# Performance work log

Hardware: AMD Instinct MI355X
Metric: run time of the kernel (lower is better)

## Reference

```python
import jax, jax.numpy as jnp
import numpy as np

DIM = 1024
HEADS = 16
HEAD_DIM = DIM // HEADS
EPS = 1e-5


def setup_inputs() -> dict:
    key = jax.random.key(0)
    ks = jax.random.split(key, 4)
    N, L = 4, 2048
    x = jax.random.normal(ks[0], (N, L, DIM), dtype=jnp.float32)
    # causal mask: True means masked (strictly upper triangle)
    attn_mask = jnp.triu(jnp.ones((L, L), dtype=jnp.bool_), k=1)[None, None, :, :]
    w_qkv = jax.random.normal(ks[1], (3 * DIM, DIM), dtype=jnp.float32) * (DIM ** -0.5)
    w_proj = jax.random.normal(ks[2], (DIM, DIM), dtype=jnp.float32) * (DIM ** -0.5)
    b_proj = jnp.zeros((DIM,), dtype=jnp.float32)
    q_gamma = jnp.ones((HEAD_DIM,), dtype=jnp.float32)
    q_beta = jnp.zeros((HEAD_DIM,), dtype=jnp.float32)
    k_gamma = jnp.ones((HEAD_DIM,), dtype=jnp.float32)
    k_beta = jnp.zeros((HEAD_DIM,), dtype=jnp.float32)
    return {"x": x, "attn_mask": attn_mask, "w_qkv": w_qkv, "w_proj": w_proj,
            "b_proj": b_proj, "q_gamma": q_gamma, "q_beta": q_beta,
            "k_gamma": k_gamma, "k_beta": k_beta}


def _layernorm(h, gamma, beta):
    mu = jnp.mean(h, axis=-1, keepdims=True)
    var = jnp.mean(jnp.square(h - mu), axis=-1, keepdims=True)
    return (h - mu) * jax.lax.rsqrt(var + EPS) * gamma + beta


def reference(x, attn_mask, w_qkv, w_proj, b_proj, q_gamma, q_beta, k_gamma, k_beta):
    N, L, D = x.shape
    H, hd = HEADS, HEAD_DIM
    scale = hd ** -0.5
    qkv = jnp.einsum('nld,ed->nle', x, w_qkv)  # [N, L, 3D]
    qkv = qkv.reshape(N, L, 3, H, hd).transpose(2, 0, 3, 1, 4)  # [3, N, H, L, hd]
    q, k, v = qkv[0], qkv[1], qkv[2]
    q = _layernorm(q, q_gamma, q_beta)
    k = _layernorm(k, k_gamma, k_beta)
    scores = jnp.einsum('nhqd,nhkd->nhqk', q * scale, k)
    scores = scores + jnp.where(attn_mask, -jnp.inf, 0.0).astype(scores.dtype)
    attn = jax.nn.softmax(scores, axis=-1)
    out = jnp.einsum('nhqk,nhkd->nhqd', attn, v)  # [N, H, L, hd]
    out = out.transpose(0, 2, 1, 3).reshape(N, L, D)
    return jnp.einsum('nld,ed->nle', out, w_proj) + b_proj
```

## Files before the change

### kernel.cpp

```cpp
#include <hip/hip_runtime.h>


using f16x8 = __attribute__((ext_vector_type(8))) _Float16;
using f16x4 = __attribute__((ext_vector_type(4))) _Float16;
using f16x2 = __attribute__((ext_vector_type(2))) _Float16;
using f32x4 = __attribute__((ext_vector_type(4))) float;
using f32x16 = __attribute__((ext_vector_type(16))) float;
using u32x4 = __attribute__((ext_vector_type(4))) unsigned int;

#define MFMA16(a, b, c) __builtin_amdgcn_mfma_f32_16x16x32_f16(a, b, c, 0, 0, 0)
#define MFMA32(a, b, c) __builtin_amdgcn_mfma_f32_32x32x16_f16(a, b, c, 0, 0, 0)

__device__ __forceinline__ void gload_lds16(const void* g, void* l) {
  __builtin_amdgcn_global_load_lds(
      (const __attribute__((address_space(1))) unsigned int*)g,
      (__attribute__((address_space(3))) unsigned int*)l, 16, 0, 0);
}

__device__ __forceinline__ float dot2acc(unsigned int pk, float c) {
#if __has_builtin(__builtin_amdgcn_fdot2)
  const f16x2 ones = {(_Float16)1.f, (_Float16)1.f};
  return __builtin_amdgcn_fdot2(__builtin_bit_cast(f16x2, pk), ones, c, false);
#else
  f16x2 v = __builtin_bit_cast(f16x2, pk);
  return c + (float)v[0] + (float)v[1];
#endif
}

__global__ __launch_bounds__(256) void f32_to_f16_kernel(
    const float* __restrict__ in, _Float16* __restrict__ out, int n) {
  int i = (blockIdx.x * 256 + threadIdx.x) * 8;
  if (i >= n) return;
  float4 a = *(const float4*)(in + i);
  float4 b = *(const float4*)(in + i + 4);
  f16x8 o;
  o[0] = (_Float16)a.x; o[1] = (_Float16)a.y; o[2] = (_Float16)a.z; o[3] = (_Float16)a.w;
  o[4] = (_Float16)b.x; o[5] = (_Float16)b.y; o[6] = (_Float16)b.z; o[7] = (_Float16)b.w;
  *(f16x8*)(out + i) = o;
}

template <int MODE>
__global__ __launch_bounds__(256) void gemm_bt(
    const _Float16* __restrict__ A, const _Float16* __restrict__ B,
    void* __restrict__ Cout, _Float16* __restrict__ Vt,
    const float* __restrict__ bias,
    const float* __restrict__ qg, const float* __restrict__ qb,
    const float* __restrict__ kg, const float* __restrict__ kb,
    int M, int N, int K) {
  __shared__ __align__(16) _Float16 As[128 * 32];
  __shared__ __align__(16) _Float16 Bs[128 * 32];
  const int tid = threadIdx.x;
  const int w = tid >> 6, lane = tid & 63;
  const int c = lane & 15, g = lane >> 4;
  const long mbase = (long)blockIdx.x * 128;
  const long nbase = (long)blockIdx.y * 128;
  const int wm = (w >> 1) * 64, wn = (w & 1) * 64;
  const int srow = w * 32 + (lane >> 2);
  const int scol = (lane & 3) * 8;

  f32x4 acc[4][4];
#pragma unroll
  for (int i = 0; i < 4; ++i)
#pragma unroll
    for (int j = 0; j < 4; ++j) acc[i][j] = f32x4{0.f, 0.f, 0.f, 0.f};

  for (int kt = 0; kt < K; kt += 32) {
    __syncthreads();
    gload_lds16(A + (mbase + srow) * K + kt + scol, As + w * 1024);
    gload_lds16(A + (mbase + srow + 16) * K + kt + scol, As + w * 1024 + 512);
    gload_lds16(B + (nbase + srow) * K + kt + scol, Bs + w * 1024);
    gload_lds16(B + (nbase + srow + 16) * K + kt + scol, Bs + w * 1024 + 512);
    __syncthreads();
    f16x8 af[4], bfr[4];
#pragma unroll
    for (int mt = 0; mt < 4; ++mt)
      af[mt] = *(const f16x8*)(As + (wm + mt * 16 + c) * 32 + g * 8);
#pragma unroll
    for (int nt = 0; nt < 4; ++nt)
      bfr[nt] = *(const f16x8*)(Bs + (wn + nt * 16 + c) * 32 + g * 8);
#pragma unroll
    for (int mt = 0; mt < 4; ++mt)
#pragma unroll
      for (int nt = 0; nt < 4; ++nt)
        acc[mt][nt] = MFMA16(af[mt], bfr[nt], acc[mt][nt]);
  }

  if constexpr (MODE == 1) {
    const int region = (int)(nbase >> 10);
    if (region == 2) {
#pragma unroll
      for (int nt = 0; nt < 4; ++nt) {
        const int dg = (int)(nbase + wn) + nt * 16 + c - 2048;
        const long vrow = ((mbase >> 11) * 16 + (dg >> 6)) * 64 + (dg & 63);
#pragma unroll
        for (int mt = 0; mt < 4; ++mt) {
          const long l0 = (mbase & 2047) + wm + mt * 16 + g * 4;
          f16x4 o;
#pragma unroll
          for (int r = 0; r < 4; ++r) o[r] = (_Float16)acc[mt][nt][r];
          *(f16x4*)(Vt + vrow * 2048 + l0) = o;
        }
      }
      return;
    }
    const float* gamma = region ? kg : qg;
    const float* beta = region ? kb : qb;
    float gam[4], bet[4];
#pragma unroll
    for (int nt = 0; nt < 4; ++nt) {
      gam[nt] = gamma[nt * 16 + c];
      bet[nt] = beta[nt * 16 + c];
    }
    const float sc = region ? 1.f : 0.1803368801111204f;
#pragma unroll
    for (int mt = 0; mt < 4; ++mt)
#pragma unroll
      for (int r = 0; r < 4; ++r) {
        float s1 = 0.f, s2 = 0.f;
#pragma unroll
        for (int nt = 0; nt < 4; ++nt) {
          const float v = acc[mt][nt][r];
          s1 += v;
          s2 += v * v;
        }
#pragma unroll
        for (int msk = 1; msk < 16; msk <<= 1) {
          s1 += __shfl_xor(s1, msk);
          s2 += __shfl_xor(s2, msk);
        }
        const float mu = s1 * 0.015625f;
        const float rstd = rsqrtf(s2 * 0.015625f - mu * mu + 1e-5f);
#pragma unroll
        for (int nt = 0; nt < 4; ++nt)
          acc[mt][nt][r] =
              ((acc[mt][nt][r] - mu) * rstd * gam[nt] + bet[nt]) * sc;
      }
#pragma unroll
    for (int nt = 0; nt < 4; ++nt) {
      const long col = nbase + wn + nt * 16 + c;
#pragma unroll
      for (int mt = 0; mt < 4; ++mt)
#pragma unroll
        for (int r = 0; r < 4; ++r) {
          const long row = mbase + wm + mt * 16 + g * 4 + r;
          ((_Float16*)Cout)[row * N + col] = (_Float16)acc[mt][nt][r];
        }
    }
  } else {
#pragma unroll
    for (int nt = 0; nt < 4; ++nt) {
      const long col = nbase + wn + nt * 16 + c;
      const float bv = bias ? bias[col] : 0.f;
#pragma unroll
      for (int mt = 0; mt < 4; ++mt)
#pragma unroll
        for (int r = 0; r < 4; ++r) {
          const long row = mbase + wm + mt * 16 + g * 4 + r;
          ((float*)Cout)[row * N + col] = acc[mt][nt][r] + bv;
        }
    }
  }
}

__global__ __launch_bounds__(256) void attn_kernel(
    const _Float16* __restrict__ qkv, const _Float16* __restrict__ Vt,
    _Float16* __restrict__ Ob) {
  __shared__ __align__(16) _Float16 Ks[2][64 * 64];
  __shared__ __align__(16) _Float16 Vs[2][64 * 64];
  const int w = threadIdx.x >> 6;
  const int lane = threadIdx.x & 63;
  const int c5 = lane & 31;
  const int hi = lane >> 5;
  const int nh = blockIdx.x;
  const long n = nh >> 4;
  const int h = nh & 15;
  const int qtile = 15 - blockIdx.y;
  const int qlo_blk = qtile * 128;
  const int qlo = qlo_blk + w * 32;
  const int qrow = qlo + c5;

  const _Float16* Qp = qkv + n * 2048 * 3072 + h * 64;
  const _Float16* Kq = Qp + 1024;
  const _Float16* Vp = Vt + (long)nh * 64 * 2048;

  const int sr8 = lane >> 3;
  const int scol = ((lane & 7) ^ sr8) * 8;

  const int nkv_blk = (qlo_blk + 191) >> 6;
  const int nkv_w = (qlo + 95) >> 6;

  const float NEG_M = -12.0f;

#define STAGE(buf, kv)                                                        \
  {                                                                           \
    const int kb_ = (kv) * 64;                                                \
    _Pragma("unroll") for (int i = 0; i < 2; ++i) {                           \
      const int idx = w * 2 + i;                                              \
      const int row = idx * 8 + sr8;                                          \
      gload_lds16(Kq + (long)(kb_ + row) * 3072 + scol, &Ks[buf][idx * 512]); \
      gload_lds16(Vp + (long)row * 2048 + kb_ + scol, &Vs[buf][idx * 512]);   \
    }                                                                         \
  }

  f16x8 qf[4];
#pragma unroll
  for (int dc = 0; dc < 4; ++dc)
    qf[dc] = *(const f16x8*)(Qp + (long)qrow * 3072 + dc * 16 + hi * 8);

  f32x16 acc[2];
#pragma unroll
  for (int db = 0; db < 2; ++db)
#pragma unroll
    for (int r = 0; r < 16; ++r) acc[db][r] = 0.f;
  float ls = 0.f;

  STAGE(0, 0);

  const int swr = c5 & 7;

  for (int kv = 0; kv < nkv_blk; ++kv) {
    const int cur = kv & 1;
    __syncthreads();
    if (kv + 1 < nkv_blk) STAGE(cur ^ 1, kv + 1);

    if (kv < nkv_w) {
      const int kbase = kv * 64;
      const _Float16* Kb = Ks[cur];
      const _Float16* Vb = Vs[cur];
      f32x16 s0, s1;
#pragma unroll
      for (int r = 0; r < 16; ++r) { s0[r] = NEG_M; s1[r] = NEG_M; }
      __builtin_amdgcn_s_setprio(1);
#pragma unroll
      for (int dc = 0; dc < 4; ++dc) {
        const int b = (dc * 2 + hi) ^ swr;
        f16x8 kf0 = *(const f16x8*)(Kb + c5 * 64 + b * 8);
        f16x8 kf1 = *(const f16x8*)(Kb + (32 + c5) * 64 + b * 8);
        s0 = MFMA32(kf0, qf[dc], s0);
        s1 = MFMA32(kf1, qf[dc], s1);
      }
      __builtin_amdgcn_s_setprio(0);
      if (kbase + 63 > qlo) {
#pragma unroll
        for (int r = 0; r < 16; ++r) {
          const int mv = (r & 3) + 8 * (r >> 2) + 4 * hi;
          if (kbase + mv > qrow) s0[r] = -1e30f;
          if (kbase + 32 + mv > qrow) s1[r] = -1e30f;
        }
      }
#pragma unroll
      for (int r = 0; r < 16; ++r) {
        s0[r] = exp2f(s0[r]);
        s1[r] = exp2f(s1[r]);
      }
      unsigned int pk0[4][2], pk1[4][2];
#pragma unroll
      for (int r2 = 0; r2 < 4; ++r2)
#pragma unroll
        for (int p = 0; p < 2; ++p) {
          pk0[r2][p] = __builtin_bit_cast(
              unsigned int,
              __builtin_amdgcn_cvt_pkrtz(s0[4 * r2 + 2 * p], s0[4 * r2 + 2 * p + 1]));
          pk1[r2][p] = __builtin_bit_cast(
              unsigned int,
              __builtin_amdgcn_cvt_pkrtz(s1[4 * r2 + 2 * p], s1[4 * r2 + 2 * p + 1]));
        }
#pragma unroll
      for (int r2 = 0; r2 < 4; ++r2)
#pragma unroll
        for (int p = 0; p < 2; ++p) {
          ls = dot2acc(pk0[r2][p], ls);
          ls = dot2acc(pk1[r2][p], ls);
        }
      f16x8 pB[4];
#pragma unroll
      for (int kk = 0; kk < 4; ++kk) {
        const int rx = (kk & 1) * 2;
        unsigned int x0 = (kk < 2) ? pk0[rx][0] : pk1[rx][0];
        unsigned int y0 = (kk < 2) ? pk0[rx + 1][0] : pk1[rx + 1][0];
        unsigned int x1 = (kk < 2) ? pk0[rx][1] : pk1[rx][1];
        unsigned int y1 = (kk < 2) ? pk0[rx + 1][1] : pk1[rx + 1][1];
        asm("v_permlane32_swap_b32 %0, %1" : "+v"(x0), "+v"(y0));
        asm("v_permlane32_swap_b32 %0, %1" : "+v"(x1), "+v"(y1));
        pB[kk] = __builtin_bit_cast(f16x8, u32x4{x0, x1, y0, y1});
      }
      __builtin_amdgcn_s_setprio(1);
#pragma unroll
      for (int db = 0; db < 2; ++db)
#pragma unroll
        for (int kk = 0; kk < 4; ++kk) {
          const int rowd = db * 32 + c5;
          const int bb = (kk * 2 + hi) ^ swr;
          f16x8 vf = *(const f16x8*)(Vb + rowd * 64 + bb * 8);
          acc[db] = MFMA32(vf, pB[kk], acc[db]);
        }
      __builtin_amdgcn_s_setprio(0);
    }
  }
  const float lsr = ls + __shfl_xor(ls, 32);
  const float inv = 1.f / lsr;
  _Float16* ob = Ob + ((long)(n * 2048) + qrow) * 1024 + h * 64 + 4 * hi;
#pragma unroll
  for (int db = 0; db < 2; ++db)
#pragma unroll
    for (int r2 = 0; r2 < 4; ++r2) {
      f16x4 o;
#pragma unroll
      for (int j = 0; j < 4; ++j)
        o[j] = (_Float16)(acc[db][4 * r2 + j] * inv);
      *(f16x4*)(ob + db * 32 + 8 * r2) = o;
    }
#undef STAGE
}

extern "C" void kernel_launch(void* const* d_in, const int* in_sizes, int n_in,
                              void* d_out, int out_size, void* d_ws, size_t ws_size,
                              hipStream_t stream) {
  const float* x = (const float*)d_in[0];
  const float* w_qkv = (const float*)d_in[2];
  const float* w_proj = (const float*)d_in[3];
  const float* b_proj = (const float*)d_in[4];
  const float* qg = (const float*)d_in[5];
  const float* qb = (const float*)d_in[6];
  const float* kg = (const float*)d_in[7];
  const float* kb = (const float*)d_in[8];

  char* ws = (char*)d_ws;
  _Float16* xb     = (_Float16*)(ws + 0);
  _Float16* wqkvb  = (_Float16*)(ws + 16777216);
  _Float16* wprojb = (_Float16*)(ws + 23068672);
  _Float16* qkvh   = (_Float16*)(ws + 25165824);
  _Float16* Vt     = (_Float16*)(ws + 75497472);
  _Float16* Ob     = xb;

  f32_to_f16_kernel<<<4096, 256, 0, stream>>>(x, xb, 8388608);
  f32_to_f16_kernel<<<1536, 256, 0, stream>>>(w_qkv, wqkvb, 3145728);
  f32_to_f16_kernel<<<512, 256, 0, stream>>>(w_proj, wprojb, 1048576);

  gemm_bt<1><<<dim3(64, 24), 256, 0, stream>>>(xb, wqkvb, qkvh, Vt, nullptr,
                                               qg, qb, kg, kb, 8192, 3072, 1024);
  attn_kernel<<<dim3(64, 16), 256, 0, stream>>>(qkvh, Vt, Ob);
  gemm_bt<0><<<dim3(64, 8), 256, 0, stream>>>(Ob, wprojb, d_out, nullptr, b_proj,
                                              nullptr, nullptr, nullptr, nullptr,
                                              8192, 1024, 1024);
}
```

Baseline: 223.1 us.

## Swizzle GEMM LDS tiles and move V transpose into separate kernel

The GEMM's LDS tiles get an XOR swizzle on the column chunk for both the global-to-LDS load and the fragment reads, meant to reduce bank conflicts on the f16x8 reads. The V slice is now written plainly into the qkv buffer by the fused QKV GEMM. A new LDS-tiled transpose kernel then builds Vt, replacing the scattered 8-byte transposed stores in the GEMM epilogue. This costs an extra kernel launch and an extra read and write of V.

```diff
diff --git a/kernel.cpp b/kernel.cpp
--- a/kernel.cpp
+++ b/kernel.cpp
@@ -42,8 +42,7 @@
 template <int MODE>
 __global__ __launch_bounds__(256) void gemm_bt(
     const _Float16* __restrict__ A, const _Float16* __restrict__ B,
-    void* __restrict__ Cout, _Float16* __restrict__ Vt,
-    const float* __restrict__ bias,
+    void* __restrict__ Cout, const float* __restrict__ bias,
     const float* __restrict__ qg, const float* __restrict__ qb,
     const float* __restrict__ kg, const float* __restrict__ kb,
     int M, int N, int K) {
@@ -56,7 +55,8 @@
   const long nbase = (long)blockIdx.y * 128;
   const int wm = (w >> 1) * 64, wn = (w & 1) * 64;
   const int srow = w * 32 + (lane >> 2);
-  const int scol = (lane & 3) * 8;
+  const int scol = ((lane & 3) ^ ((lane >> 3) & 3)) * 8;
+  const int sg = (g ^ ((c >> 1) & 3)) * 8;
 
   f32x4 acc[4][4];
 #pragma unroll
@@ -74,10 +74,10 @@
     f16x8 af[4], bfr[4];
 #pragma unroll
     for (int mt = 0; mt < 4; ++mt)
-      af[mt] = *(const f16x8*)(As + (wm + mt * 16 + c) * 32 + g * 8);
+      af[mt] = *(const f16x8*)(As + (wm + mt * 16 + c) * 32 + sg);
 #pragma unroll
     for (int nt = 0; nt < 4; ++nt)
-      bfr[nt] = *(const f16x8*)(Bs + (wn + nt * 16 + c) * 32 + g * 8);
+      bfr[nt] = *(const f16x8*)(Bs + (wn + nt * 16 + c) * 32 + sg);
 #pragma unroll
     for (int mt = 0; mt < 4; ++mt)
 #pragma unroll
@@ -87,54 +87,40 @@
 
   if constexpr (MODE == 1) {
     const int region = (int)(nbase >> 10);
-    if (region == 2) {
+    if (region < 2) {
+      const float* gamma = region ? kg : qg;
+      const float* beta = region ? kb : qb;
+      float gam[4], bet[4];
 #pragma unroll
       for (int nt = 0; nt < 4; ++nt) {
-        const int dg = (int)(nbase + wn) + nt * 16 + c - 2048;
-        const long vrow = ((mbase >> 11) * 16 + (dg >> 6)) * 64 + (dg & 63);
-#pragma unroll
-        for (int mt = 0; mt < 4; ++mt) {
-          const long l0 = (mbase & 2047) + wm + mt * 16 + g * 4;
-          f16x4 o;
-#pragma unroll
-          for (int r = 0; r < 4; ++r) o[r] = (_Float16)acc[mt][nt][r];
-          *(f16x4*)(Vt + vrow * 2048 + l0) = o;
-        }
-      }
-      return;
-    }
-    const float* gamma = region ? kg : qg;
-    const float* beta = region ? kb : qb;
-    float gam[4], bet[4];
-#pragma unroll
-    for (int nt = 0; nt < 4; ++nt) {
-      gam[nt] = gamma[nt * 16 + c];
-      bet[nt] = beta[nt * 16 + c];
-    }
-    const float sc = region ? 1.f : 0.1803368801111204f;
-#pragma unroll
-    for (int mt = 0; mt < 4; ++mt)
-#pragma unroll
-      for (int r = 0; r < 4; ++r) {
-        float s1 = 0.f, s2 = 0.f;
-#pragma unroll
-        for (int nt = 0; nt < 4; ++nt) {
-          const float v = acc[mt][nt][r];
-          s1 += v;
-          s2 += v * v;
-        }
-#pragma unroll
-        for (int msk = 1; msk < 16; msk <<= 1) {
-          s1 += __shfl_xor(s1, msk);
-          s2 += __shfl_xor(s2, msk);
-        }
-        const float mu = s1 * 0.015625f;
-        const float rstd = rsqrtf(s2 * 0.015625f - mu * mu + 1e-5f);
-#pragma unroll
-        for (int nt = 0; nt < 4; ++nt)
-          acc[mt][nt][r] =
-              ((acc[mt][nt][r] - mu) * rstd * gam[nt] + bet[nt]) * sc;
-      }
+        gam[nt] = gamma[nt * 16 + c];
+        bet[nt] = beta[nt * 16 + c];
+      }
+      const float sc = region ? 1.f : 0.1803368801111204f;
+#pragma unroll
+      for (int mt = 0; mt < 4; ++mt)
+#pragma unroll
+        for (int r = 0; r < 4; ++r) {
+          float s1 = 0.f, s2 = 0.f;
+#pragma unroll
+          for (int nt = 0; nt < 4; ++nt) {
+            const float v = acc[mt][nt][r];
+            s1 += v;
+            s2 += v * v;
+          }
+#pragma unroll
+          for (int msk = 1; msk < 16; msk <<= 1) {
+            s1 += __shfl_xor(s1, msk);
+            s2 += __shfl_xor(s2, msk);
+          }
+          const float mu = s1 * 0.015625f;
+          const float rstd = rsqrtf(s2 * 0.015625f - mu * mu + 1e-5f);
+#pragma unroll
+          for (int nt = 0; nt < 4; ++nt)
+            acc[mt][nt][r] =
+                ((acc[mt][nt][r] - mu) * rstd * gam[nt] + bet[nt]) * sc;
+        }
+    }
 #pragma unroll
     for (int nt = 0; nt < 4; ++nt) {
       const long col = nbase + wn + nt * 16 + c;
@@ -160,6 +146,34 @@
         }
     }
   }
+}
+
+__global__ __launch_bounds__(256) void transpose_v_kernel(
+    const _Float16* __restrict__ qkv, _Float16* __restrict__ Vt) {
+  __shared__ __align__(16) _Float16 tile[64][80];
+  const int nh = blockIdx.y;
+  const long n = nh >> 4;
+  const int h = nh & 15;
+  const long lbase = (long)blockIdx.x * 64;
+  const int t = threadIdx.x;
+#pragma unroll
+  for (int r = 0; r < 2; ++r) {
+    const int l = (t + r * 256) >> 3;
+    const int cc = (t & 7) * 8;
+    f16x8 v = *(const f16x8*)(qkv + (n * 2048 + lbase + l) * 3072 + 2048 + h * 64 + cc);
+    *(f16x8*)&tile[l][cc] = v;
+  }
+  __syncthreads();
+  const int d = t >> 2, q = t & 3;
+  f16x8 o0, o1;
+#pragma unroll
+  for (int i = 0; i < 8; ++i) {
+    o0[i] = tile[q * 16 + i][d];
+    o1[i] = tile[q * 16 + 8 + i][d];
+  }
+  _Float16* dst = Vt + ((long)nh * 64 + d) * 2048 + lbase + q * 16;
+  *(f16x8*)dst = o0;
+  *(f16x8*)(dst + 8) = o1;
 }
 
 __global__ __launch_bounds__(256) void attn_kernel(
@@ -337,10 +351,11 @@
   f32_to_f16_kernel<<<1536, 256, 0, stream>>>(w_qkv, wqkvb, 3145728);
   f32_to_f16_kernel<<<512, 256, 0, stream>>>(w_proj, wprojb, 1048576);
 
-  gemm_bt<1><<<dim3(64, 24), 256, 0, stream>>>(xb, wqkvb, qkvh, Vt, nullptr,
+  gemm_bt<1><<<dim3(64, 24), 256, 0, stream>>>(xb, wqkvb, qkvh, nullptr,
                                                qg, qb, kg, kb, 8192, 3072, 1024);
+  transpose_v_kernel<<<dim3(32, 64), 256, 0, stream>>>(qkvh, Vt);
   attn_kernel<<<dim3(64, 16), 256, 0, stream>>>(qkvh, Vt, Ob);
-  gemm_bt<0><<<dim3(64, 8), 256, 0, stream>>>(Ob, wprojb, d_out, nullptr, b_proj,
+  gemm_bt<0><<<dim3(64, 8), 256, 0, stream>>>(Ob, wprojb, d_out, b_proj,
                                               nullptr, nullptr, nullptr, nullptr,
                                               8192, 1024, 1024);
 }
```

After: 214.9 us. 1.04x faster.
